# Kernel tuning notes

Hardware: AMD Instinct MI355X
Metric: run time of the kernel (lower is better)

Reference implementation:

```python
import jax, jax.numpy as jnp
import numpy as np
import math

B, L, E, H, K = 4, 1024, 1024, 16, 64
D = E // H  # head_dim = 64; rel_pe has 2K+1 = 129 rows


def setup_inputs() -> dict:
    key = jax.random.key(0)
    ks = jax.random.split(key, 4)
    s = 1.0 / math.sqrt(E)
    return {
        "q": jax.random.normal(ks[0], (B, L, E), dtype=jnp.float32),
        "in_proj_weight": jax.random.normal(ks[1], (3 * E, E), dtype=jnp.float32) * s,
        "in_proj_bias": jnp.zeros((3 * E,), dtype=jnp.float32),
        "out_w": jax.random.normal(ks[2], (E, E), dtype=jnp.float32) * s,
        "out_b": jnp.zeros((E,), dtype=jnp.float32),
        "rel_pe": jax.random.normal(ks[3], (2 * K + 1, D), dtype=jnp.float32) * (1.0 / math.sqrt(D)),
    }


def _attend(q, in_proj_weight, in_proj_bias, out_w, out_b, rel_pe):
    b, l, e = q.shape
    h, d = H, D
    qkv = q @ in_proj_weight.T + in_proj_bias  # (B, L, 3E)
    qh, kh, vh = jnp.split(qkv, 3, axis=-1)
    # (B, L, E) -> (B, H, L, D)
    qh = qh.reshape(b, l, h, d).transpose(0, 2, 1, 3)
    kh = kh.reshape(b, l, h, d).transpose(0, 2, 1, 3)
    vh = vh.reshape(b, l, h, d).transpose(0, 2, 1, 3)
    qh = qh / math.sqrt(d)  # scaling applies to both content and position terms
    # content scores
    scores = jnp.einsum("bhid,bhjd->bhij", qh, kh)
    # relative-position bias: a[i, j] = rel_pe[clip(j - i, -K, K) + K]
    # compute q . rel_pe once, then gather per (i, j) -- same math as the
    # original O(L^2 * D) materialized tensor, without building it.
    pos = jnp.arange(l)
    rel = jnp.clip(pos[None, :] - pos[:, None], -K, K) + K  # (L, L) int
    bias_r = jnp.einsum("bhid,rd->bhir", qh, rel_pe)  # (B, H, L, 2K+1)
    bias = jnp.take_along_axis(bias_r, jnp.broadcast_to(rel[None, None], (b, h, l, l)), axis=-1)
    attn = jax.nn.softmax(scores + bias, axis=-1)
    out = jnp.einsum("bhij,bhjd->bhid", attn, vh)  # (B, H, L, D)
    out = out.transpose(0, 2, 1, 3).reshape(b, l, e)
    return out @ out_w.T + out_b


def reference(q, in_proj_weight, in_proj_bias, out_w, out_b, rel_pe):
    return _attend(q, in_proj_weight, in_proj_bias, out_w, out_b, rel_pe)
```

## Files before the change

### kernel.cpp

```cpp
#include <hip/hip_runtime.h>
#include <math.h>

typedef _Float16 half_t;
typedef _Float16 half8 __attribute__((ext_vector_type(8)));
typedef _Float16 half4v __attribute__((ext_vector_type(4)));
typedef float float4v __attribute__((ext_vector_type(4)));
typedef float float16v __attribute__((ext_vector_type(16)));

#define AS1 __attribute__((address_space(1)))
#define AS3 __attribute__((address_space(3)))

#define MFMA16(a, b, c) __builtin_amdgcn_mfma_f32_16x16x32_f16((a), (b), (c), 0, 0, 0)
#define MFMA32(a, b, c) __builtin_amdgcn_mfma_f32_32x32x16_f16((a), (b), (c), 0, 0, 0)

#define QSCALE 0.18033688f
#define TABOFF 2.88539008f

__device__ __forceinline__ void gload16(const half_t* g, half_t* l) {
    __builtin_amdgcn_global_load_lds((const AS1 void*)g, (AS3 void*)l, 16, 0, 0);
}

__device__ __forceinline__ int iclamp(int v, int lo, int hi) {
    return v < lo ? lo : (v > hi ? hi : v);
}

__device__ __forceinline__ unsigned pkrtz_bits(float a, float b) {
    auto w = __builtin_amdgcn_cvt_pkrtz(a, b);
    unsigned u;
    __builtin_memcpy(&u, &w, 4);
    return u;
}

__global__ __launch_bounds__(256) void cast_kernel(
    const float* __restrict__ q, const float* __restrict__ w_in,
    const float* __restrict__ w_out, const float* __restrict__ pe,
    half_t* __restrict__ q16, half_t* __restrict__ w16,
    half_t* __restrict__ wo16, half_t* __restrict__ pe16)
{
    const int tid = blockIdx.x * 256 + threadIdx.x;
    const int stride = gridDim.x * 256;
    for (int i = tid; i < 1048576; i += stride) {
        float4 v = ((const float4*)q)[i];
        *(half4v*)(q16 + (size_t)i * 4) =
            (half4v){(half_t)v.x, (half_t)v.y, (half_t)v.z, (half_t)v.w};
    }
    for (int i = tid; i < 786432; i += stride) {
        float4 v = ((const float4*)w_in)[i];
        *(half4v*)(w16 + (size_t)i * 4) =
            (half4v){(half_t)v.x, (half_t)v.y, (half_t)v.z, (half_t)v.w};
    }
    for (int i = tid; i < 262144; i += stride) {
        float4 v = ((const float4*)w_out)[i];
        *(half4v*)(wo16 + (size_t)i * 4) =
            (half4v){(half_t)v.x, (half_t)v.y, (half_t)v.z, (half_t)v.w};
    }
    for (int i = tid; i < 2064; i += stride) {
        float4 v = ((const float4*)pe)[i];
        *(half4v*)(pe16 + (size_t)i * 4) =
            (half4v){(half_t)v.x, (half_t)v.y, (half_t)v.z, (half_t)v.w};
    }
    for (int i = tid; i < 496; i += stride) {
        *(half4v*)(pe16 + 8256 + (size_t)i * 4) = (half4v){0, 0, 0, 0};
    }
}

__global__ __launch_bounds__(256) void qkv_gemm(
    const half_t* __restrict__ A, const half_t* __restrict__ W,
    const float* __restrict__ bias,
    half_t* __restrict__ qh, half_t* __restrict__ kh, half_t* __restrict__ vt)
{
    __shared__ half_t As[128 * 32];
    __shared__ half_t Bs[128 * 32];
    const int K = 1024;
    const int tid = threadIdx.x, lane = tid & 63, wid = tid >> 6;
    const int wm = wid & 1, wn = wid >> 1;
    const int bid = blockIdx.x;
    const int xcd = bid & 7, idx = bid >> 3;
    const int m0 = (((xcd >> 1) << 3) + (idx & 7)) * 128;
    const int n0 = (((xcd & 1) * 12) + (idx >> 3)) * 128;

    const half_t* gA[2]; const half_t* gB[2];
    half_t* lA[2]; half_t* lB[2];
    {
        const int base = wid * 128;
#pragma unroll
        for (int c = 0; c < 2; ++c) {
            int slot = base + c * 64 + lane;
            int row = slot >> 2;
            int ch = (slot & 3) ^ ((row >> 1) & 3);
            gA[c] = A + (size_t)(m0 + row) * K + ch * 8;
            gB[c] = W + (size_t)(n0 + row) * K + ch * 8;
            lA[c] = As + (base + c * 64) * 8;
            lB[c] = Bs + (base + c * 64) * 8;
        }
    }
    int aOff[4], bOff[4];
#pragma unroll
    for (int i = 0; i < 4; ++i) {
        int ra = wm * 64 + i * 16 + (lane & 15);
        aOff[i] = ra * 32 + (((lane >> 4) ^ ((ra >> 1) & 3)) * 8);
        int rb = wn * 64 + i * 16 + (lane & 15);
        bOff[i] = rb * 32 + (((lane >> 4) ^ ((rb >> 1) & 3)) * 8);
    }
    float4v acc[4][4];
#pragma unroll
    for (int i = 0; i < 4; ++i)
#pragma unroll
        for (int j = 0; j < 4; ++j) acc[i][j] = (float4v){0.f, 0.f, 0.f, 0.f};

    for (int k0 = 0; k0 < K; k0 += 32) {
        __syncthreads();
        gload16(gA[0], lA[0]); gload16(gA[1], lA[1]);
        gload16(gB[0], lB[0]); gload16(gB[1], lB[1]);
        gA[0] += 32; gA[1] += 32; gB[0] += 32; gB[1] += 32;
        __syncthreads();
        half8 af[4], bf[4];
#pragma unroll
        for (int i = 0; i < 4; ++i) af[i] = *(const half8*)(As + aOff[i]);
#pragma unroll
        for (int j = 0; j < 4; ++j) bf[j] = *(const half8*)(Bs + bOff[j]);
#pragma unroll
        for (int i = 0; i < 4; ++i)
#pragma unroll
            for (int j = 0; j < 4; ++j)
                acc[i][j] = MFMA16(af[i], bf[j], acc[i][j]);
    }

    const int part = n0 >> 10;
#pragma unroll
    for (int ni = 0; ni < 4; ++ni) {
        const int col = n0 + wn * 64 + ni * 16 + (lane & 15);
        const float bv = bias[col];
        const int hh = (col >> 6) & 15, d = col & 63;
#pragma unroll
        for (int mi = 0; mi < 4; ++mi) {
            const int r0 = m0 + wm * 64 + mi * 16 + ((lane >> 4) << 2);
            const int bb = r0 >> 10, l0 = r0 & 1023;
            if (part == 0) {
#pragma unroll
                for (int r = 0; r < 4; ++r)
                    qh[(((size_t)(bb * 16 + hh) * 1024) + l0 + r) * 64 + d] =
                        (half_t)((acc[mi][ni][r] + bv) * QSCALE);
            } else if (part == 1) {
#pragma unroll
                for (int r = 0; r < 4; ++r)
                    kh[(((size_t)(bb * 16 + hh) * 1024) + l0 + r) * 64 + d] =
                        (half_t)(acc[mi][ni][r] + bv);
            } else {
                half4v pk;
#pragma unroll
                for (int r = 0; r < 4; ++r) pk[r] = (half_t)(acc[mi][ni][r] + bv);
                *(half4v*)(vt + ((size_t)(bb * 16 + hh) * 64 + d) * 1024 + l0) = pk;
            }
        }
    }
}

__global__ __launch_bounds__(256) void out_gemm(
    const half_t* __restrict__ A, const half_t* __restrict__ W,
    const float* __restrict__ bias, float* __restrict__ C)
{
    __shared__ half_t As[128 * 32];
    __shared__ half_t Bs[64 * 32];
    const int K = 1024;
    const int tid = threadIdx.x, lane = tid & 63, wid = tid >> 6;
    const int wm = wid & 1, wn = wid >> 1;
    const int bid = blockIdx.x;
    const int xcd = bid & 7, idx = bid >> 3;
    const int m0 = ((xcd << 2) + (idx >> 4)) * 128;
    const int n0 = (idx & 15) * 64;

    const half_t* gA[2]; const half_t* gB1;
    half_t* lA[2]; half_t* lB1;
    {
        const int base = wid * 128;
#pragma unroll
        for (int c = 0; c < 2; ++c) {
            int slot = base + c * 64 + lane;
            int row = slot >> 2;
            int ch = (slot & 3) ^ ((row >> 1) & 3);
            gA[c] = A + (size_t)(m0 + row) * K + ch * 8;
            lA[c] = As + (base + c * 64) * 8;
        }
        int slotB = wid * 64 + lane;
        int rowB = slotB >> 2;
        int chB = (slotB & 3) ^ ((rowB >> 1) & 3);
        gB1 = W + (size_t)(n0 + rowB) * K + chB * 8;
        lB1 = Bs + (wid * 64) * 8;
    }
    int aOff[4], bOff[2];
#pragma unroll
    for (int i = 0; i < 4; ++i) {
        int ra = wm * 64 + i * 16 + (lane & 15);
        aOff[i] = ra * 32 + (((lane >> 4) ^ ((ra >> 1) & 3)) * 8);
    }
#pragma unroll
    for (int j = 0; j < 2; ++j) {
        int rb = wn * 32 + j * 16 + (lane & 15);
        bOff[j] = rb * 32 + (((lane >> 4) ^ ((rb >> 1) & 3)) * 8);
    }
    float4v acc[4][2];
#pragma unroll
    for (int i = 0; i < 4; ++i)
#pragma unroll
        for (int j = 0; j < 2; ++j) acc[i][j] = (float4v){0.f, 0.f, 0.f, 0.f};

    for (int k0 = 0; k0 < K; k0 += 32) {
        __syncthreads();
        gload16(gA[0], lA[0]); gload16(gA[1], lA[1]);
        gload16(gB1, lB1);
        gA[0] += 32; gA[1] += 32; gB1 += 32;
        __syncthreads();
        half8 af[4], bf[2];
#pragma unroll
        for (int i = 0; i < 4; ++i) af[i] = *(const half8*)(As + aOff[i]);
#pragma unroll
        for (int j = 0; j < 2; ++j) bf[j] = *(const half8*)(Bs + bOff[j]);
#pragma unroll
        for (int i = 0; i < 4; ++i)
#pragma unroll
            for (int j = 0; j < 2; ++j)
                acc[i][j] = MFMA16(af[i], bf[j], acc[i][j]);
    }

#pragma unroll
    for (int ni = 0; ni < 2; ++ni) {
        const int col = n0 + wn * 32 + ni * 16 + (lane & 15);
        const float bv = bias[col];
#pragma unroll
        for (int mi = 0; mi < 4; ++mi) {
            const int r0 = m0 + wm * 64 + mi * 16 + ((lane >> 4) << 2);
#pragma unroll
            for (int r = 0; r < 4; ++r)
                C[(size_t)(r0 + r) * 1024 + col] = acc[mi][ni][r] + bv;
        }
    }
}

__global__ __launch_bounds__(256) void attn_mfma(
    const half_t* __restrict__ qh, const half_t* __restrict__ kh,
    const half_t* __restrict__ vt, const half_t* __restrict__ pe,
    half_t* __restrict__ ao)
{
    __shared__ half_t KV[2 * 8192];
    __shared__ half_t R2[4 * 32 * 172];

    const int tid = threadIdx.x, lane = tid & 63, wid = tid >> 6;
    const int hl = lane >> 5, ql = lane & 31;
    const int bid = blockIdx.x;
    const int xcd = bid & 7, idx = bid >> 3;
    const int bh = xcd + ((idx >> 3) << 3);
    const int q0 = (idx & 7) * 128;
    const int h = bh & 15, b = bh >> 4;
    const int i0w = q0 + wid * 32;
    const int i0w_s = __builtin_amdgcn_readfirstlane(i0w);
    const size_t hbase = (size_t)(b * 16 + h) * 64 * 1024;
    const half_t* Qg = qh + hbase;
    const half_t* Kg = kh + hbase;
    const half_t* Vg = vt + hbase;

    const half_t* gS[4]; int lOff[4]; int ginc[4];
#pragma unroll
    for (int c = 0; c < 4; ++c) {
        const int slot0 = wid * 256 + c * 64;
        const int slot = slot0 + lane;
        if (slot0 < 512) {
            int srow = slot >> 3, sch = (slot & 7) ^ (srow & 7);
            gS[c] = Kg + srow * 64 + sch * 8;
            ginc[c] = 64 * 64;
            lOff[c] = slot0 * 8;
        } else {
            int s2 = slot - 512;
            int srow = s2 >> 3, sch = (s2 & 7) ^ (srow & 7);
            gS[c] = Vg + srow * 1024 + sch * 8;
            ginc[c] = 64;
            lOff[c] = 4096 + (slot0 - 512) * 8;
        }
    }

#pragma unroll
    for (int c = 0; c < 4; ++c) { gload16(gS[c], KV + lOff[c]); gS[c] += ginc[c]; }

    const int qrow = i0w + ql;
    half8 qb[4];
#pragma unroll
    for (int cc = 0; cc < 4; ++cc)
        qb[cc] = *(const half8*)(Qg + (size_t)qrow * 64 + cc * 16 + hl * 8);

    half_t* r2w = R2 + wid * (32 * 172);
#pragma unroll
    for (int j2 = 0; j2 < 5; ++j2) {
        float16v c;
#pragma unroll
        for (int r = 0; r < 16; ++r) c[r] = 0.f;
#pragma unroll
        for (int cc = 0; cc < 4; ++cc) {
            half8 pb = *(const half8*)(pe + (size_t)(j2 * 32 + ql) * 64 + cc * 16 + hl * 8);
            c = MFMA32(qb[cc], pb, c);
        }
        const int col = j2 * 32 + ql;
        if (col < 129) {
#pragma unroll
            for (int reg = 0; reg < 16; ++reg) {
                const int il = (reg & 3) + 8 * (reg >> 2) + 4 * hl;
                const half_t hv = (half_t)(c[reg] - TABOFF);
                if (col == 0) {
                    for (int ts = 0; ts <= il + 4; ++ts) r2w[il * 172 + ts] = hv;
                } else if (col == 128) {
                    for (int ts = il + 132; ts <= il + 139; ++ts) r2w[il * 172 + ts] = hv;
                } else {
                    r2w[il * 172 + col + 4 + il] = hv;
                }
            }
        }
    }
    asm volatile("s_waitcnt lgkmcnt(0)" ::: "memory");

    const half_t* r2row = r2w + ql * 172;

    const float c_lo = (float)r2row[0];
    const float c_hi = (float)r2row[ql + 132];
    float16v s_lo_init, s_hi_init;
#pragma unroll
    for (int r = 0; r < 16; ++r) { s_lo_init[r] = c_lo; s_hi_init[r] = c_hi; }

    int kOff[2][4], vOff[2][4];
#pragma unroll
    for (int t2 = 0; t2 < 2; ++t2)
#pragma unroll
        for (int cc = 0; cc < 4; ++cc) {
            int row = t2 * 32 + ql;
            int ch = (cc * 2 + hl) ^ (row & 7);
            kOff[t2][cc] = row * 64 + ch * 8;
            vOff[t2][cc] = 4096 + row * 64 + ch * 8;
        }

    const int hiC = 128 + ((ql + 3) & ~3);

    float4v lacc = (float4v){0.f, 0.f, 0.f, 0.f};
    float16v oacc[2];
#pragma unroll
    for (int dt = 0; dt < 2; ++dt)
#pragma unroll
        for (int r = 0; r < 16; ++r) oacc[dt][r] = 0.f;

    for (int kt2 = 0; kt2 < 8; ++kt2) {
#pragma unroll
        for (int kk = 0; kk < 2; ++kk) {
            const int kt = kt2 * 2 + kk;
            if (kt < 15) {
#pragma unroll
                for (int c = 0; c < 4; ++c) {
                    gload16(gS[c], KV + (kk ^ 1) * 8192 + lOff[c]);
                    gS[c] += ginc[c];
                }
                asm volatile("s_waitcnt vmcnt(4)" ::: "memory");
            } else {
                asm volatile("s_waitcnt vmcnt(0)" ::: "memory");
            }
            __builtin_amdgcn_s_barrier();
            asm volatile("" ::: "memory");

            const half_t* KVb = KV + kk * 8192;
            const int kt64 = kt << 6;
            const bool far_hi = (kt64 >= i0w_s + 95);
            const bool far_lo = (kt64 <= i0w_s - 127);

            unsigned pw[2][4][2];
#pragma unroll
            for (int t2 = 0; t2 < 2; ++t2) {
                float16v s;
                if (far_hi) {
                    s = s_hi_init;
                } else if (far_lo) {
                    s = s_lo_init;
                } else {
#pragma unroll
                    for (int g = 0; g < 4; ++g) {
                        int traw = kt64 + t2 * 32 + 8 * g + 4 * hl + 64 - i0w;
                        int tsb = iclamp(traw, -4, hiC) + 4;
                        half4v bh4 = *(const half4v*)(r2row + tsb);
#pragma unroll
                        for (int r = 0; r < 4; ++r) s[4 * g + r] = (float)bh4[r];
                    }
                }
#pragma unroll
                for (int cc = 0; cc < 4; ++cc) {
                    half8 kf = *(const half8*)(KVb + kOff[t2][cc]);
                    s = MFMA32(kf, qb[cc], s);
                }
#pragma unroll
                for (int g = 0; g < 4; ++g) {
                    float p0 = __builtin_amdgcn_exp2f(s[4 * g + 0]);
                    float p1 = __builtin_amdgcn_exp2f(s[4 * g + 1]);
                    float p2 = __builtin_amdgcn_exp2f(s[4 * g + 2]);
                    float p3 = __builtin_amdgcn_exp2f(s[4 * g + 3]);
                    lacc += (float4v){p0, p1, p2, p3};
                    pw[t2][g][0] = pkrtz_bits(p0, p1);
                    pw[t2][g][1] = pkrtz_bits(p2, p3);
                }
            }

            half8 pf[4];
#pragma unroll
            for (int cc = 0; cc < 4; ++cc) {
                const int t2c = cc >> 1, ge = (cc & 1) * 2;
                auto r0 = __builtin_amdgcn_permlane32_swap(
                    pw[t2c][ge][0], pw[t2c][ge + 1][0], false, false);
                auto r1 = __builtin_amdgcn_permlane32_swap(
                    pw[t2c][ge][1], pw[t2c][ge + 1][1], false, false);
                unsigned pfw[4] = {r0[0], r1[0], r0[1], r1[1]};
                __builtin_memcpy(&pf[cc], pfw, 16);
            }

#pragma unroll
            for (int dt = 0; dt < 2; ++dt)
#pragma unroll
                for (int cc = 0; cc < 4; ++cc) {
                    half8 vf = *(const half8*)(KVb + vOff[dt][cc]);
                    oacc[dt] = MFMA32(vf, pf[cc], oacc[dt]);
                }

            asm volatile("" ::: "memory");
            __builtin_amdgcn_s_barrier();
        }
    }

    float l_r = lacc[0] + lacc[1] + lacc[2] + lacc[3];
    l_r += __shfl_xor(l_r, 32);
    const float inv = 1.0f / l_r;

    half_t* aorow = ao + ((size_t)(b * 1024 + i0w + ql)) * 1024 + h * 64;
#pragma unroll
    for (int dt = 0; dt < 2; ++dt)
#pragma unroll
        for (int g = 0; g < 4; ++g) {
            const int d0 = dt * 32 + 8 * g + 4 * hl;
            half4v oh;
#pragma unroll
            for (int r = 0; r < 4; ++r) oh[r] = (half_t)(oacc[dt][4 * g + r] * inv);
            *(half4v*)(aorow + d0) = oh;
        }
}

extern "C" void kernel_launch(void* const* d_in, const int* in_sizes, int n_in,
                              void* d_out, int out_size, void* d_ws, size_t ws_size,
                              hipStream_t stream) {
    const float* q     = (const float*)d_in[0];
    const float* w_in  = (const float*)d_in[1];
    const float* b_in  = (const float*)d_in[2];
    const float* w_out = (const float*)d_in[3];
    const float* b_out = (const float*)d_in[4];
    const float* pe    = (const float*)d_in[5];
    float* out = (float*)d_out;

    half_t* ws = (half_t*)d_ws;
    half_t* q16   = ws;
    half_t* w16   = q16 + 4194304;
    half_t* wo16  = w16 + 3145728;
    half_t* pe16  = wo16 + 1048576;
    half_t* qh16  = pe16 + 10240;
    half_t* kh16  = qh16 + 4194304;
    half_t* vt16  = kh16 + 4194304;
    half_t* ao16  = vt16 + 4194304;

    cast_kernel<<<2048, 256, 0, stream>>>(q, w_in, w_out, pe, q16, w16, wo16, pe16);
    qkv_gemm<<<768, 256, 0, stream>>>(q16, w16, b_in, qh16, kh16, vt16);
    attn_mfma<<<512, 256, 0, stream>>>(qh16, kh16, vt16, pe16, ao16);
    out_gemm<<<512, 256, 0, stream>>>(ao16, wo16, b_out, out);
}
```

Measured before the change: 176.1 us.

## Software-pipeline attention loop: compute next QK^T while doing current PV

```diff
diff --git a/kernel.cpp b/kernel.cpp
--- a/kernel.cpp
+++ b/kernel.cpp
@@ -29,6 +29,60 @@
     unsigned u;
     __builtin_memcpy(&u, &w, 4);
     return u;
+}
+
+__device__ __forceinline__ void softmax_pack(const float16v* s, float4v& lacc,
+                                             half8* pf) {
+    unsigned pw[2][4][2];
+#pragma unroll
+    for (int t2 = 0; t2 < 2; ++t2)
+#pragma unroll
+        for (int g = 0; g < 4; ++g) {
+            float p0 = __builtin_amdgcn_exp2f(s[t2][4 * g + 0]);
+            float p1 = __builtin_amdgcn_exp2f(s[t2][4 * g + 1]);
+            float p2 = __builtin_amdgcn_exp2f(s[t2][4 * g + 2]);
+            float p3 = __builtin_amdgcn_exp2f(s[t2][4 * g + 3]);
+            lacc += (float4v){p0, p1, p2, p3};
+            pw[t2][g][0] = pkrtz_bits(p0, p1);
+            pw[t2][g][1] = pkrtz_bits(p2, p3);
+        }
+#pragma unroll
+    for (int cc = 0; cc < 4; ++cc) {
+        const int t2c = cc >> 1, ge = (cc & 1) * 2;
+        auto r0 = __builtin_amdgcn_permlane32_swap(
+            pw[t2c][ge][0], pw[t2c][ge + 1][0], false, false);
+        auto r1 = __builtin_amdgcn_permlane32_swap(
+            pw[t2c][ge][1], pw[t2c][ge + 1][1], false, false);
+        unsigned pfw[4] = {r0[0], r1[0], r0[1], r1[1]};
+        __builtin_memcpy(&pf[cc], pfw, 16);
+    }
+}
+
+__device__ __forceinline__ void bias_init(int kt64, int i0w, int i0w_s, int hl,
+                                          int hiC, const half_t* r2row,
+                                          float c_lo, float c_hi, float16v* s) {
+    if (kt64 >= i0w_s + 95) {
+#pragma unroll
+        for (int t2 = 0; t2 < 2; ++t2)
+#pragma unroll
+            for (int r = 0; r < 16; ++r) s[t2][r] = c_hi;
+    } else if (kt64 <= i0w_s - 127) {
+#pragma unroll
+        for (int t2 = 0; t2 < 2; ++t2)
+#pragma unroll
+            for (int r = 0; r < 16; ++r) s[t2][r] = c_lo;
+    } else {
+#pragma unroll
+        for (int t2 = 0; t2 < 2; ++t2)
+#pragma unroll
+            for (int g = 0; g < 4; ++g) {
+                int traw = kt64 + t2 * 32 + 8 * g + 4 * hl + 64 - i0w;
+                int tsb = iclamp(traw, -4, hiC) + 4;
+                half4v bh4 = *(const half4v*)(r2row + tsb);
+#pragma unroll
+                for (int r = 0; r < 4; ++r) s[t2][4 * g + r] = (float)bh4[r];
+            }
+    }
 }
 
 __global__ __launch_bounds__(256) void cast_kernel(
@@ -237,7 +291,7 @@
     }
 }
 
-__global__ __launch_bounds__(256) void attn_mfma(
+__global__ __launch_bounds__(256, 2) void attn_mfma(
     const half_t* __restrict__ qh, const half_t* __restrict__ kh,
     const half_t* __restrict__ vt, const half_t* __restrict__ pe,
     half_t* __restrict__ ao)
@@ -280,6 +334,8 @@
 
 #pragma unroll
     for (int c = 0; c < 4; ++c) { gload16(gS[c], KV + lOff[c]); gS[c] += ginc[c]; }
+#pragma unroll
+    for (int c = 0; c < 4; ++c) { gload16(gS[c], KV + 8192 + lOff[c]); gS[c] += ginc[c]; }
 
     const int qrow = i0w + ql;
     half8 qb[4];
@@ -317,12 +373,9 @@
     asm volatile("s_waitcnt lgkmcnt(0)" ::: "memory");
 
     const half_t* r2row = r2w + ql * 172;
-
     const float c_lo = (float)r2row[0];
     const float c_hi = (float)r2row[ql + 132];
-    float16v s_lo_init, s_hi_init;
-#pragma unroll
-    for (int r = 0; r < 16; ++r) { s_lo_init[r] = c_lo; s_hi_init[r] = c_hi; }
+    const int hiC = 128 + ((ql + 3) & ~3);
 
     int kOff[2][4], vOff[2][4];
 #pragma unroll
@@ -335,8 +388,6 @@
             vOff[t2][cc] = 4096 + row * 64 + ch * 8;
         }
 
-    const int hiC = 128 + ((ql + 3) & ~3);
-
     float4v lacc = (float4v){0.f, 0.f, 0.f, 0.f};
     float16v oacc[2];
 #pragma unroll
@@ -344,86 +395,75 @@
 #pragma unroll
         for (int r = 0; r < 16; ++r) oacc[dt][r] = 0.f;
 
-    for (int kt2 = 0; kt2 < 8; ++kt2) {
-#pragma unroll
-        for (int kk = 0; kk < 2; ++kk) {
-            const int kt = kt2 * 2 + kk;
-            if (kt < 15) {
-#pragma unroll
-                for (int c = 0; c < 4; ++c) {
-                    gload16(gS[c], KV + (kk ^ 1) * 8192 + lOff[c]);
-                    gS[c] += ginc[c];
-                }
-                asm volatile("s_waitcnt vmcnt(4)" ::: "memory");
-            } else {
-                asm volatile("s_waitcnt vmcnt(0)" ::: "memory");
+    asm volatile("s_waitcnt vmcnt(0)" ::: "memory");
+    __builtin_amdgcn_s_barrier();
+
+    half8 pf[4];
+    {
+        float16v s[2];
+        bias_init(0, i0w, i0w_s, hl, hiC, r2row, c_lo, c_hi, s);
+#pragma unroll
+        for (int t2 = 0; t2 < 2; ++t2)
+#pragma unroll
+            for (int cc = 0; cc < 4; ++cc) {
+                half8 kf = *(const half8*)(KV + kOff[t2][cc]);
+                s[t2] = MFMA32(kf, qb[cc], s[t2]);
             }
-            __builtin_amdgcn_s_barrier();
-            asm volatile("" ::: "memory");
-
-            const half_t* KVb = KV + kk * 8192;
-            const int kt64 = kt << 6;
-            const bool far_hi = (kt64 >= i0w_s + 95);
-            const bool far_lo = (kt64 <= i0w_s - 127);
-
-            unsigned pw[2][4][2];
-#pragma unroll
-            for (int t2 = 0; t2 < 2; ++t2) {
-                float16v s;
-                if (far_hi) {
-                    s = s_hi_init;
-                } else if (far_lo) {
-                    s = s_lo_init;
-                } else {
-#pragma unroll
-                    for (int g = 0; g < 4; ++g) {
-                        int traw = kt64 + t2 * 32 + 8 * g + 4 * hl + 64 - i0w;
-                        int tsb = iclamp(traw, -4, hiC) + 4;
-                        half4v bh4 = *(const half4v*)(r2row + tsb);
-#pragma unroll
-                        for (int r = 0; r < 4; ++r) s[4 * g + r] = (float)bh4[r];
-                    }
-                }
-#pragma unroll
-                for (int cc = 0; cc < 4; ++cc) {
-                    half8 kf = *(const half8*)(KVb + kOff[t2][cc]);
-                    s = MFMA32(kf, qb[cc], s);
-                }
-#pragma unroll
-                for (int g = 0; g < 4; ++g) {
-                    float p0 = __builtin_amdgcn_exp2f(s[4 * g + 0]);
-                    float p1 = __builtin_amdgcn_exp2f(s[4 * g + 1]);
-                    float p2 = __builtin_amdgcn_exp2f(s[4 * g + 2]);
-                    float p3 = __builtin_amdgcn_exp2f(s[4 * g + 3]);
-                    lacc += (float4v){p0, p1, p2, p3};
-                    pw[t2][g][0] = pkrtz_bits(p0, p1);
-                    pw[t2][g][1] = pkrtz_bits(p2, p3);
-                }
+        softmax_pack(s, lacc, pf);
+    }
+
+    for (int kt = 0; kt < 16; ++kt) {
+        asm volatile("s_waitcnt vmcnt(0)" ::: "memory");
+        __builtin_amdgcn_s_barrier();
+
+        const half_t* bufN = KV + (((kt + 1) & 1) << 13);
+        const half_t* bufC = KV + ((kt & 1) << 13);
+        const bool hasn = kt < 15;
+
+        half8 kfn[2][4], vf[2][4];
+        if (hasn) {
+#pragma unroll
+            for (int t2 = 0; t2 < 2; ++t2)
+#pragma unroll
+                for (int cc = 0; cc < 4; ++cc)
+                    kfn[t2][cc] = *(const half8*)(bufN + kOff[t2][cc]);
+        }
+#pragma unroll
+        for (int dt = 0; dt < 2; ++dt)
+#pragma unroll
+            for (int cc = 0; cc < 4; ++cc)
+                vf[dt][cc] = *(const half8*)(bufC + vOff[dt][cc]);
+
+        float16v s[2];
+        if (hasn)
+            bias_init((kt + 1) << 6, i0w, i0w_s, hl, hiC, r2row, c_lo, c_hi, s);
+
+        asm volatile("s_waitcnt lgkmcnt(0)" ::: "memory");
+        __builtin_amdgcn_s_barrier();
+
+        if (kt < 14) {
+#pragma unroll
+            for (int c = 0; c < 4; ++c) {
+                gload16(gS[c], KV + ((kt & 1) << 13) + lOff[c]);
+                gS[c] += ginc[c];
             }
-
-            half8 pf[4];
-#pragma unroll
-            for (int cc = 0; cc < 4; ++cc) {
-                const int t2c = cc >> 1, ge = (cc & 1) * 2;
-                auto r0 = __builtin_amdgcn_permlane32_swap(
-                    pw[t2c][ge][0], pw[t2c][ge + 1][0], false, false);
-                auto r1 = __builtin_amdgcn_permlane32_swap(
-                    pw[t2c][ge][1], pw[t2c][ge + 1][1], false, false);
-                unsigned pfw[4] = {r0[0], r1[0], r0[1], r1[1]};
-                __builtin_memcpy(&pf[cc], pfw, 16);
-            }
-
-#pragma unroll
-            for (int dt = 0; dt < 2; ++dt)
-#pragma unroll
-                for (int cc = 0; cc < 4; ++cc) {
-                    half8 vf = *(const half8*)(KVb + vOff[dt][cc]);
-                    oacc[dt] = MFMA32(vf, pf[cc], oacc[dt]);
-                }
-
-            asm volatile("" ::: "memory");
-            __builtin_amdgcn_s_barrier();
-        }
+        }
+
+        if (hasn) {
+#pragma unroll
+            for (int t2 = 0; t2 < 2; ++t2)
+#pragma unroll
+                for (int cc = 0; cc < 4; ++cc)
+                    s[t2] = MFMA32(kfn[t2][cc], qb[cc], s[t2]);
+        }
+
+#pragma unroll
+        for (int dt = 0; dt < 2; ++dt)
+#pragma unroll
+            for (int cc = 0; cc < 4; ++cc)
+                oacc[dt] = MFMA32(vf[dt][cc], pf[cc], oacc[dt]);
+
+        if (hasn) softmax_pack(s, lacc, pf);
     }
 
     float l_r = lacc[0] + lacc[1] + lacc[2] + lacc[3];
```

New measurement: 208.0 us. +18.1%, slower.
